# Kernel tuning notes

Hardware: AMD Instinct MI355X
Metric: run time of the kernel (lower is better)

The kernel has to match this reference:

```python
import jax, jax.numpy as jnp
import numpy as np

NEG_INF = -1e30  # large negative for masking; avoids inf*0 NaNs under softmax


def setup_inputs() -> dict:
    key = jax.random.key(0)
    kq, kk, kv, kd = jax.random.split(key, 4)
    B, H, N, D = 1, 16, 4096, 64
    Q = jax.random.normal(kq, (B, H, N, D), dtype=jnp.float32)
    K = jax.random.normal(kk, (B, H, N, D), dtype=jnp.float32)
    V = jax.random.normal(kv, (B, H, N, D), dtype=jnp.float32)
    document_id = jnp.sort(jax.random.randint(kd, (N,), 0, 16, dtype=jnp.int32))
    return {"Q": Q, "K": K, "V": V, "document_id": document_id}


def reference(Q, K, V, document_id):
    # Q, K, V: [B, H, N, D]; document_id: [N]
    B, H, N, D = Q.shape
    scale = 1.0 / jnp.sqrt(jnp.float32(D))  # flex_attention default scaling
    # document mask: token pairs attend only within the same document
    mask = document_id[:, None] == document_id[None, :]  # [N, N] bool
    scores = jnp.einsum('bhqd,bhkd->bhqk', Q, K) * scale  # [B, H, N, N]
    scores = jnp.where(mask[None, None, :, :], scores, NEG_INF)
    probs = jax.nn.softmax(scores, axis=-1)
    out = jnp.einsum('bhqk,bhkd->bhqd', probs, V)  # [B, H, N, D]
    return out
```

## Files before the change

### kernel.cpp

```cpp
#include <hip/hip_runtime.h>
#include <hip/hip_bf16.h>

typedef __attribute__((ext_vector_type(8))) short short8;
typedef __attribute__((ext_vector_type(4))) float f32x4;
typedef __attribute__((ext_vector_type(4))) unsigned int u32x4;
typedef __attribute__((ext_vector_type(4))) unsigned short u16x4;
typedef unsigned short u16;

#define MFMA16 __builtin_amdgcn_mfma_f32_16x16x32_bf16

__device__ __forceinline__ u16 f2bf(float x) {
    unsigned int u = __builtin_bit_cast(unsigned int, x);
    u = (u + 0x7FFFu + ((u >> 16) & 1u)) >> 16;
    return (u16)u;
}

constexpr int N_TOK = 4096;
constexpr int DH = 64;
constexpr int KMAX = 128;
constexpr int KST = 72;
constexpr int VST = 136;
constexpr float SCALE = 0.125f;
constexpr float SHIFT = 8.0f;
constexpr float MASKVAL = -1e30f;

__global__ __launch_bounds__(512, 4)
void doc_attn_v16(const float* __restrict__ Qg, const float* __restrict__ Kg,
                  const float* __restrict__ Vg, const int* __restrict__ doc,
                  float* __restrict__ Out) {
    __shared__ __align__(16) u16 Klds[KMAX][KST];
    __shared__ __align__(16) u16 Vtld[DH][VST];
    __shared__ int bnd[2];

    const int bid = blockIdx.x;
    const int swz = ((bid & 7) << 7) | (bid >> 3);
    const int h = swz >> 6;
    const int dI = (swz >> 2) & 15;
    const int qq = swz & 3;
    const int tid = threadIdx.x;
    const int lane = tid & 63;
    const int w = tid >> 6;
    const int l15 = lane & 15;
    const int lg = lane >> 4;

    if (tid == 0) { bnd[0] = N_TOK; bnd[1] = N_TOK; }
    __syncthreads();
    {
        const int i0 = tid * 8;
        int prev = (i0 == 0) ? -1 : doc[i0 - 1];
        #pragma unroll
        for (int j = 0; j < 8; ++j) {
            const int cur = doc[i0 + j];
            if (cur >= dI && prev < dI) bnd[0] = i0 + j;
            if (cur >= dI + 1 && prev < dI + 1) bnd[1] = i0 + j;
            prev = cur;
        }
    }
    __syncthreads();
    const int qs = bnd[0], qe = bnd[1];
    const int len = qe - qs;
    if (len <= 0) return;

    const int nG = (len + 15) >> 4;
    const int nGq = (nG + 3) >> 2;
    const int gBeg = qq * nGq;
    const int gEnd = min(nG, gBeg + nGq);
    if (gBeg >= gEnd) return;

    const int src0 = l15 + ((lane & 16) << 1);
    const int src1 = src0 + 16;
    const bool khsel = (lg >> 1) != 0;

    for (int g0 = gBeg; g0 < gEnd; g0 += 8) {
        const int g = g0 + w;
        const int gid = (g < gEnd) ? g : -1;
        short8 aq[2];
        {
            const int gl = (g < gEnd) ? g : 0;
            const int qrow = min(qs + gl * 16 + l15, N_TOK - 1);
            const float* qp = &Qg[((size_t)h * N_TOK + qrow) * DH + lg * 8];
            #pragma unroll
            for (int kc = 0; kc < 2; ++kc) {
                float4 f0 = *(const float4*)(qp + kc * 32);
                float4 f1 = *(const float4*)(qp + kc * 32 + 4);
                short8 a;
                a[0]=(short)f2bf(f0.x*SCALE); a[1]=(short)f2bf(f0.y*SCALE);
                a[2]=(short)f2bf(f0.z*SCALE); a[3]=(short)f2bf(f0.w*SCALE);
                a[4]=(short)f2bf(f1.x*SCALE); a[5]=(short)f2bf(f1.y*SCALE);
                a[6]=(short)f2bf(f1.z*SCALE); a[7]=(short)f2bf(f1.w*SCALE);
                aq[kc] = a;
            }
        }

        f32x4 o_acc[4];
        float lsum = 0.f;
        #pragma unroll
        for (int db = 0; db < 4; ++db) o_acc[db] = (f32x4){0.f, 0.f, 0.f, 0.f};

        for (int c0 = 0; c0 < len; c0 += KMAX) {
            const int clen = min(KMAX, len - c0);
            const int ctiles = (clen + 31) >> 5;
            const int cl32 = ctiles << 5;

            __syncthreads();

            for (int idx = tid; idx < clen * 16; idx += 512) {
                const int r = idx >> 4, c = (idx & 15) * 4;
                const float4 kf = *(const float4*)&Kg[((size_t)h * N_TOK + qs + c0 + r) * DH + c];
                const float4 vf = *(const float4*)&Vg[((size_t)h * N_TOK + qs + c0 + r) * DH + c];
                u16x4 o4;
                o4[0] = f2bf(kf.x); o4[1] = f2bf(kf.y);
                o4[2] = f2bf(kf.z); o4[3] = f2bf(kf.w);
                *(u16x4*)&Klds[r][c] = o4;
                Vtld[c + 0][r] = f2bf(vf.x);
                Vtld[c + 1][r] = f2bf(vf.y);
                Vtld[c + 2][r] = f2bf(vf.z);
                Vtld[c + 3][r] = f2bf(vf.w);
            }
            for (int idx = tid; idx < DH * 32; idx += 512) {
                const int d_ = idx >> 5;
                const int col = (clen & ~31) + (idx & 31);
                if (col >= clen && col < cl32) Vtld[d_][col] = 0;
            }
            __syncthreads();

            if (gid >= 0) {
                for (int t = 0; t < ctiles; ++t) {
                    const int kb = t << 5;
                    short8 bk[2][2];
                    #pragma unroll
                    for (int kh = 0; kh < 2; ++kh)
                        #pragma unroll
                        for (int kc = 0; kc < 2; ++kc)
                            bk[kh][kc] = *(const short8*)&Klds[kb + kh * 16 + l15][lg * 8 + kc * 32];

                    f32x4 sa0 = (f32x4){-SHIFT, -SHIFT, -SHIFT, -SHIFT};
                    f32x4 sa1 = (f32x4){-SHIFT, -SHIFT, -SHIFT, -SHIFT};
                    __builtin_amdgcn_s_setprio(1);
                    sa0 = MFMA16(bk[0][0], aq[0], sa0, 0, 0, 0);
                    sa0 = MFMA16(bk[0][1], aq[1], sa0, 0, 0, 0);
                    sa1 = MFMA16(bk[1][0], aq[0], sa1, 0, 0, 0);
                    sa1 = MFMA16(bk[1][1], aq[1], sa1, 0, 0, 0);
                    __builtin_amdgcn_s_setprio(0);

                    float p0[4], p1[4];
                    #pragma unroll
                    for (int i = 0; i < 4; ++i) {
                        const int key0 = kb + lg * 4 + i;
                        const float x0 = (key0 < clen)      ? sa0[i] : MASKVAL;
                        const float x1 = (key0 + 16 < clen) ? sa1[i] : MASKVAL;
                        p0[i] = __expf(x0);
                        p1[i] = __expf(x1);
                        lsum += p0[i] + p1[i];
                    }

                    const unsigned int a0 = (unsigned int)f2bf(p0[0]) | ((unsigned int)f2bf(p0[1]) << 16);
                    const unsigned int a1 = (unsigned int)f2bf(p0[2]) | ((unsigned int)f2bf(p0[3]) << 16);
                    const unsigned int b0 = (unsigned int)f2bf(p1[0]) | ((unsigned int)f2bf(p1[1]) << 16);
                    const unsigned int b1 = (unsigned int)f2bf(p1[2]) | ((unsigned int)f2bf(p1[3]) << 16);
                    const unsigned int t00 = __shfl((int)a0, src0);
                    const unsigned int t01 = __shfl((int)a1, src0);
                    const unsigned int t10 = __shfl((int)b0, src0);
                    const unsigned int t11 = __shfl((int)b1, src0);
                    const unsigned int u00 = __shfl((int)a0, src1);
                    const unsigned int u01 = __shfl((int)a1, src1);
                    const unsigned int u10 = __shfl((int)b0, src1);
                    const unsigned int u11 = __shfl((int)b1, src1);
                    u32x4 af;
                    af[0] = khsel ? t10 : t00;
                    af[1] = khsel ? t11 : t01;
                    af[2] = khsel ? u10 : u00;
                    af[3] = khsel ? u11 : u01;
                    const short8 pa = __builtin_bit_cast(short8, af);

                    short8 bv[4];
                    #pragma unroll
                    for (int db = 0; db < 4; ++db)
                        bv[db] = *(const short8*)&Vtld[db * 16 + l15][kb + lg * 8];

                    __builtin_amdgcn_s_setprio(1);
                    #pragma unroll
                    for (int db = 0; db < 4; ++db)
                        o_acc[db] = MFMA16(bv[db], pa, o_acc[db], 0, 0, 0);
                    __builtin_amdgcn_s_setprio(0);
                }
            }
        }

        if (gid >= 0) {
            float rs = lsum;
            rs += __shfl_xor(rs, 16);
            rs += __shfl_xor(rs, 32);
            const float inv = 1.0f / rs;
            const int qrow = qs + gid * 16 + l15;
            if (qrow < qe) {
                float* op = &Out[((size_t)h * N_TOK + qrow) * DH + lg * 4];
                #pragma unroll
                for (int db = 0; db < 4; ++db) {
                    float4 v;
                    v.x = o_acc[db][0] * inv;
                    v.y = o_acc[db][1] * inv;
                    v.z = o_acc[db][2] * inv;
                    v.w = o_acc[db][3] * inv;
                    *(float4*)(op + db * 16) = v;
                }
            }
        }
        lsum = 0.f;
    }
}

extern "C" void kernel_launch(void* const* d_in, const int* in_sizes, int n_in,
                              void* d_out, int out_size, void* d_ws, size_t ws_size,
                              hipStream_t stream) {
    const float* Q = (const float*)d_in[0];
    const float* K = (const float*)d_in[1];
    const float* V = (const float*)d_in[2];
    const int* doc = (const int*)d_in[3];
    float* out = (float*)d_out;

    doc_attn_v16<<<dim3(1024), 512, 0, stream>>>(Q, K, V, doc, out);
}
```

Before: 41.59 us.

## Pre-convert K/V to bf16 in workspace and run single-wave attention blocks

```diff
diff --git a/kernel.cpp b/kernel.cpp
--- a/kernel.cpp
+++ b/kernel.cpp
@@ -17,19 +17,213 @@
 
 constexpr int N_TOK = 4096;
 constexpr int DH = 64;
-constexpr int KMAX = 128;
-constexpr int KST = 72;
-constexpr int VST = 136;
+constexpr int NH = 16;
+constexpr int NTP = N_TOK + 32;
 constexpr float SCALE = 0.125f;
 constexpr float SHIFT = 8.0f;
 constexpr float MASKVAL = -1e30f;
+
+__global__ __launch_bounds__(256)
+void doc_prep(const float* __restrict__ Kg, const float* __restrict__ Vg,
+              const int* __restrict__ doc, u16* __restrict__ Kbf,
+              u16* __restrict__ Vtb, int* __restrict__ bnds) {
+    const int b = blockIdx.x;
+    const int tid = threadIdx.x;
+    if (b < 2048) {
+        __shared__ u16 tile[DH][40];
+        const int h = b >> 7, k0 = (b & 127) * 32;
+        #pragma unroll
+        for (int i = 0; i < 2; ++i) {
+            const int idx = tid + i * 256;
+            const int r = idx >> 4, c = (idx & 15) * 4;
+            const float4 f = *(const float4*)&Vg[((size_t)h * N_TOK + k0 + r) * DH + c];
+            tile[c + 0][r] = f2bf(f.x); tile[c + 1][r] = f2bf(f.y);
+            tile[c + 2][r] = f2bf(f.z); tile[c + 3][r] = f2bf(f.w);
+        }
+        __syncthreads();
+        #pragma unroll
+        for (int i = 0; i < 2; ++i) {
+            const int idx = tid + i * 256;
+            const int d = idx >> 3, kq = (idx & 7) * 4;
+            u16x4 o;
+            o[0] = tile[d][kq + 0]; o[1] = tile[d][kq + 1];
+            o[2] = tile[d][kq + 2]; o[3] = tile[d][kq + 3];
+            *(u16x4*)&Vtb[((size_t)h * DH + d) * NTP + k0 + kq] = o;
+        }
+        if ((b & 127) == 127) {
+            for (int i = tid; i < DH * 8; i += 256) {
+                const int d = i >> 3, kq = (i & 7) * 4;
+                u16x4 z; z[0] = 0; z[1] = 0; z[2] = 0; z[3] = 0;
+                *(u16x4*)&Vtb[((size_t)h * DH + d) * NTP + N_TOK + kq] = z;
+            }
+        }
+    } else if (b < 4096) {
+        const int bb = b - 2048;
+        const int h = bb >> 7, k0 = (bb & 127) * 32;
+        #pragma unroll
+        for (int i = 0; i < 2; ++i) {
+            const int idx = tid + i * 256;
+            const int r = idx >> 4, c = (idx & 15) * 4;
+            const float4 f = *(const float4*)&Kg[((size_t)h * N_TOK + k0 + r) * DH + c];
+            u16x4 o;
+            o[0] = f2bf(f.x); o[1] = f2bf(f.y); o[2] = f2bf(f.z); o[3] = f2bf(f.w);
+            *(u16x4*)&Kbf[((size_t)h * N_TOK + k0 + r) * DH + c] = o;
+        }
+    } else {
+        if (tid < 17) bnds[tid] = N_TOK;
+        __syncthreads();
+        const int i0 = tid * 16;
+        int prev = (i0 == 0) ? -1 : doc[i0 - 1];
+        for (int j = 0; j < 16; ++j) {
+            const int cur = doc[i0 + j];
+            for (int dd = prev + 1; dd <= cur; ++dd) bnds[dd] = i0 + j;
+            prev = cur;
+        }
+    }
+}
+
+__global__ __launch_bounds__(64, 4)
+void doc_attn_v18(const float* __restrict__ Qg, const u16* __restrict__ Kbf,
+                  const u16* __restrict__ Vtb, const int* __restrict__ bnds,
+                  float* __restrict__ Out) {
+    const int b = blockIdx.x;
+    const int swz = ((b & 7) << 9) | (b >> 3);
+    const int h = swz >> 8;
+    const int dI = (swz >> 4) & 15;
+    const int slot = swz & 15;
+    const int lane = threadIdx.x;
+    const int l15 = lane & 15;
+    const int lg = lane >> 4;
+
+    const int qs = bnds[dI], qe = bnds[dI + 1];
+    const int len = qe - qs;
+    if (len <= 0) return;
+    const int nG = (len + 15) >> 4;
+    if (slot >= nG) return;
+
+    const int src0 = l15 + ((lane & 16) << 1);
+    const int src1 = src0 + 16;
+    const bool khsel = (lg >> 1) != 0;
+
+    const int abs0 = qs & ~31;
+    const int ctiles = (qe - abs0 + 31) >> 5;
+
+    for (int g = slot; g < nG; g += 16) {
+        short8 aq[2];
+        {
+            const int qrow = min(qs + g * 16 + l15, N_TOK - 1);
+            const float* qp = &Qg[((size_t)h * N_TOK + qrow) * DH + lg * 8];
+            #pragma unroll
+            for (int kc = 0; kc < 2; ++kc) {
+                float4 f0 = *(const float4*)(qp + kc * 32);
+                float4 f1 = *(const float4*)(qp + kc * 32 + 4);
+                short8 a;
+                a[0]=(short)f2bf(f0.x*SCALE); a[1]=(short)f2bf(f0.y*SCALE);
+                a[2]=(short)f2bf(f0.z*SCALE); a[3]=(short)f2bf(f0.w*SCALE);
+                a[4]=(short)f2bf(f1.x*SCALE); a[5]=(short)f2bf(f1.y*SCALE);
+                a[6]=(short)f2bf(f1.z*SCALE); a[7]=(short)f2bf(f1.w*SCALE);
+                aq[kc] = a;
+            }
+        }
+
+        f32x4 o_acc[4];
+        float lsum = 0.f;
+        #pragma unroll
+        for (int db = 0; db < 4; ++db) o_acc[db] = (f32x4){0.f, 0.f, 0.f, 0.f};
+
+        for (int t = 0; t < ctiles; ++t) {
+            const int kb = abs0 + (t << 5);
+            short8 bk[2][2];
+            #pragma unroll
+            for (int kh = 0; kh < 2; ++kh) {
+                const int kr = min(kb + kh * 16 + l15, N_TOK - 1);
+                const u16* kp = &Kbf[((size_t)h * N_TOK + kr) * DH + lg * 8];
+                bk[kh][0] = *(const short8*)(kp);
+                bk[kh][1] = *(const short8*)(kp + 32);
+            }
+
+            f32x4 sa0 = (f32x4){-SHIFT, -SHIFT, -SHIFT, -SHIFT};
+            f32x4 sa1 = (f32x4){-SHIFT, -SHIFT, -SHIFT, -SHIFT};
+            __builtin_amdgcn_s_setprio(1);
+            sa0 = MFMA16(bk[0][0], aq[0], sa0, 0, 0, 0);
+            sa0 = MFMA16(bk[0][1], aq[1], sa0, 0, 0, 0);
+            sa1 = MFMA16(bk[1][0], aq[0], sa1, 0, 0, 0);
+            sa1 = MFMA16(bk[1][1], aq[1], sa1, 0, 0, 0);
+            __builtin_amdgcn_s_setprio(0);
+
+            float p0[4], p1[4];
+            #pragma unroll
+            for (int i = 0; i < 4; ++i) {
+                const int key0 = kb + lg * 4 + i;
+                const int key1 = key0 + 16;
+                const float x0 = (key0 >= qs && key0 < qe) ? sa0[i] : MASKVAL;
+                const float x1 = (key1 >= qs && key1 < qe) ? sa1[i] : MASKVAL;
+                p0[i] = __expf(x0);
+                p1[i] = __expf(x1);
+                lsum += p0[i] + p1[i];
+            }
+
+            const unsigned int a0 = (unsigned int)f2bf(p0[0]) | ((unsigned int)f2bf(p0[1]) << 16);
+            const unsigned int a1 = (unsigned int)f2bf(p0[2]) | ((unsigned int)f2bf(p0[3]) << 16);
+            const unsigned int b0w = (unsigned int)f2bf(p1[0]) | ((unsigned int)f2bf(p1[1]) << 16);
+            const unsigned int b1w = (unsigned int)f2bf(p1[2]) | ((unsigned int)f2bf(p1[3]) << 16);
+            const unsigned int t00 = __shfl((int)a0, src0);
+            const unsigned int t01 = __shfl((int)a1, src0);
+            const unsigned int t10 = __shfl((int)b0w, src0);
+            const unsigned int t11 = __shfl((int)b1w, src0);
+            const unsigned int u00 = __shfl((int)a0, src1);
+            const unsigned int u01 = __shfl((int)a1, src1);
+            const unsigned int u10 = __shfl((int)b0w, src1);
+            const unsigned int u11 = __shfl((int)b1w, src1);
+            u32x4 af;
+            af[0] = khsel ? t10 : t00;
+            af[1] = khsel ? t11 : t01;
+            af[2] = khsel ? u10 : u00;
+            af[3] = khsel ? u11 : u01;
+            const short8 pa = __builtin_bit_cast(short8, af);
+
+            short8 bv[4];
+            #pragma unroll
+            for (int db = 0; db < 4; ++db)
+                bv[db] = *(const short8*)&Vtb[((size_t)h * DH + db * 16 + l15) * NTP + kb + lg * 8];
+
+            __builtin_amdgcn_s_setprio(1);
+            #pragma unroll
+            for (int db = 0; db < 4; ++db)
+                o_acc[db] = MFMA16(bv[db], pa, o_acc[db], 0, 0, 0);
+            __builtin_amdgcn_s_setprio(0);
+        }
+
+        float rs = lsum;
+        rs += __shfl_xor(rs, 16);
+        rs += __shfl_xor(rs, 32);
+        const float inv = 1.0f / rs;
+        const int qrow = qs + g * 16 + l15;
+        if (qrow < qe) {
+            float* op = &Out[((size_t)h * N_TOK + qrow) * DH + lg * 4];
+            #pragma unroll
+            for (int db = 0; db < 4; ++db) {
+                float4 v;
+                v.x = o_acc[db][0] * inv;
+                v.y = o_acc[db][1] * inv;
+                v.z = o_acc[db][2] * inv;
+                v.w = o_acc[db][3] * inv;
+                *(float4*)(op + db * 16) = v;
+            }
+        }
+    }
+}
+
+constexpr int KMAXF = 128;
+constexpr int KSTF = 72;
+constexpr int VSTF = 136;
 
 __global__ __launch_bounds__(512, 4)
 void doc_attn_v16(const float* __restrict__ Qg, const float* __restrict__ Kg,
                   const float* __restrict__ Vg, const int* __restrict__ doc,
                   float* __restrict__ Out) {
-    __shared__ __align__(16) u16 Klds[KMAX][KST];
-    __shared__ __align__(16) u16 Vtld[DH][VST];
+    __shared__ __align__(16) u16 Klds[KMAXF][KSTF];
+    __shared__ __align__(16) u16 Vtld[DH][VSTF];
     __shared__ int bnd[2];
 
     const int bid = blockIdx.x;
@@ -97,8 +291,8 @@
         #pragma unroll
         for (int db = 0; db < 4; ++db) o_acc[db] = (f32x4){0.f, 0.f, 0.f, 0.f};
 
-        for (int c0 = 0; c0 < len; c0 += KMAX) {
-            const int clen = min(KMAX, len - c0);
+        for (int c0 = 0; c0 < len; c0 += KMAXF) {
+            const int clen = min(KMAXF, len - c0);
             const int ctiles = (clen + 31) >> 5;
             const int cl32 = ctiles << 5;
 
@@ -156,16 +350,16 @@
 
                     const unsigned int a0 = (unsigned int)f2bf(p0[0]) | ((unsigned int)f2bf(p0[1]) << 16);
                     const unsigned int a1 = (unsigned int)f2bf(p0[2]) | ((unsigned int)f2bf(p0[3]) << 16);
-                    const unsigned int b0 = (unsigned int)f2bf(p1[0]) | ((unsigned int)f2bf(p1[1]) << 16);
-                    const unsigned int b1 = (unsigned int)f2bf(p1[2]) | ((unsigned int)f2bf(p1[3]) << 16);
+                    const unsigned int b0w = (unsigned int)f2bf(p1[0]) | ((unsigned int)f2bf(p1[1]) << 16);
+                    const unsigned int b1w = (unsigned int)f2bf(p1[2]) | ((unsigned int)f2bf(p1[3]) << 16);
                     const unsigned int t00 = __shfl((int)a0, src0);
                     const unsigned int t01 = __shfl((int)a1, src0);
-                    const unsigned int t10 = __shfl((int)b0, src0);
-                    const unsigned int t11 = __shfl((int)b1, src0);
+                    const unsigned int t10 = __shfl((int)b0w, src0);
+                    const unsigned int t11 = __shfl((int)b1w, src0);
                     const unsigned int u00 = __shfl((int)a0, src1);
                     const unsigned int u01 = __shfl((int)a1, src1);
-                    const unsigned int u10 = __shfl((int)b0, src1);
-                    const unsigned int u11 = __shfl((int)b1, src1);
+                    const unsigned int u10 = __shfl((int)b0w, src1);
+                    const unsigned int u11 = __shfl((int)b1w, src1);
                     u32x4 af;
                     af[0] = khsel ? t10 : t00;
                     af[1] = khsel ? t11 : t01;
@@ -219,5 +413,18 @@
     const int* doc = (const int*)d_in[3];
     float* out = (float*)d_out;
 
-    doc_attn_v16<<<dim3(1024), 512, 0, stream>>>(Q, K, V, doc, out);
+    const size_t kbf_bytes = (size_t)NH * N_TOK * DH * 2;
+    const size_t vtb_bytes = (size_t)NH * DH * NTP * 2;
+    const size_t bnds_off = kbf_bytes + vtb_bytes;
+    const size_t need = bnds_off + 256;
+
+    if (ws_size >= need) {
+        u16* Kbf = (u16*)d_ws;
+        u16* Vtb = (u16*)((char*)d_ws + kbf_bytes);
+        int* bnds = (int*)((char*)d_ws + bnds_off);
+        doc_prep<<<dim3(4097), 256, 0, stream>>>(K, V, doc, Kbf, Vtb, bnds);
+        doc_attn_v18<<<dim3(4096), 64, 0, stream>>>(Q, Kbf, Vtb, bnds, out);
+    } else {
+        doc_attn_v16<<<dim3(1024), 512, 0, stream>>>(Q, K, V, doc, out);
+    }
 }
```

Measured after the change: 64.57 us. +55.3%, slower.
